# Kernel optimization log

Measured on AMD Instinct MI355X. Metric: run time of the kernel, lower is better.

The kernel has to match this reference:

```python
import jax, jax.numpy as jnp
import numpy as np

N = 50000        # nodes
E = 800000       # edges (avg degree 16)
MUL = 32         # multiplicity of 0e and 1o node-feature irreps
NA = 16          # node attr scalars (species embedding)
NB = 8           # edge radial basis size
FC_H = 64        # radial MLP hidden width
NPATH = 5        # tp paths: 0e*0e->0e, 0e*1o->1o, 1o*0e->1o, 1o*1o->0e, 1o*1o->1o
AVG_NEI = 16.0


def setup_inputs() -> dict:
    k = jax.random.split(jax.random.key(0), 16)
    return dict(
        node_feats=jax.random.normal(k[0], (N, 4 * MUL), jnp.float32),   # 32x0e + 32x1o
        node_attrs=jax.random.normal(k[1], (N, NA), jnp.float32),
        edge_embedding=jax.random.uniform(k[2], (E, NB), jnp.float32),
        edge_attrs=jax.random.normal(k[3], (E, 4), jnp.float32),         # SH l=0 (1) + l=1 (3)
        edge_src=jax.random.randint(k[4], (E,), 0, N),
        edge_dst=jax.random.randint(k[5], (E,), 0, N),
        W1_s=jax.random.normal(k[6], (MUL, MUL), jnp.float32) / np.sqrt(MUL),
        W1_v=jax.random.normal(k[7], (MUL, MUL), jnp.float32) / np.sqrt(MUL),
        fc_w1=jax.random.normal(k[8], (NB, FC_H), jnp.float32) / np.sqrt(NB),
        fc_b1=jnp.zeros((FC_H,), jnp.float32),
        fc_w2=jax.random.normal(k[9], (FC_H, NPATH * MUL), jnp.float32) / np.sqrt(FC_H),
        W2_s=jax.random.normal(k[10], (2 * MUL, 2 * MUL), jnp.float32) / np.sqrt(2 * MUL),
        W2_v=jax.random.normal(k[11], (3 * MUL, MUL), jnp.float32) / np.sqrt(3 * MUL),
        Wsc_s=jax.random.normal(k[12], (MUL, NA, 2 * MUL), jnp.float32) / np.sqrt(MUL * NA),
        Wsc_v=jax.random.normal(k[13], (MUL, NA, MUL), jnp.float32) / np.sqrt(MUL * NA),
    )


def reference(node_feats, node_attrs, edge_embedding, edge_attrs,
              edge_src, edge_dst, W1_s, W1_v, fc_w1, fc_b1, fc_w2,
              W2_s, W2_v, Wsc_s, Wsc_v):
    n = node_feats.shape[0]
    s = node_feats[:, :MUL]                        # [N, mul]     0e scalars
    v = node_feats[:, MUL:].reshape(n, MUL, 3)     # [N, mul, 3]  1o vectors

    # linear_1: per-irrep multiplicity mixing
    x_s = s @ W1_s
    x_v = jnp.einsum('nuc,uv->nvc', v, W1_v)

    # radial network -> per-edge tensor-product path weights (uvu, mul_in2 = 1)
    w = jax.nn.silu(edge_embedding @ fc_w1 + fc_b1) @ fc_w2   # [E, 5*mul]
    w00, w01, w10, w11s, w11v = [w[:, i * MUL:(i + 1) * MUL] for i in range(NPATH)]

    sh0 = edge_attrs[:, :1]     # [E, 1]  l=0
    sh1 = edge_attrs[:, 1:4]    # [E, 3]  l=1

    xs = x_s[edge_src]          # [E, mul]      gather source-node features
    xv = x_v[edge_src]          # [E, mul, 3]

    # Clebsch-Gordan tensor-product messages
    m_s0 = w00 * xs * sh0                                              # 0e x 0e -> 0e
    m_s1 = w11s * jnp.einsum('euc,ec->eu', xv, sh1) / np.sqrt(3.0)     # 1o x 1o -> 0e
    m_v0 = (w01 * xs)[:, :, None] * sh1[:, None, :]                    # 0e x 1o -> 1o
    m_v1 = w10[:, :, None] * xv * sh0[:, :, None]                      # 1o x 0e -> 1o
    m_v2 = w11v[:, :, None] * jnp.cross(
        xv, jnp.broadcast_to(sh1[:, None, :], xv.shape)) / np.sqrt(2.0)  # 1o x 1o -> 1o

    # scatter-sum to destination nodes, normalized by sqrt(avg num neighbors)
    inv = 1.0 / np.sqrt(AVG_NEI)
    a_s = jax.ops.segment_sum(jnp.concatenate([m_s0, m_s1], axis=1),
                              edge_dst, num_segments=n) * inv           # [N, 2*mul]
    a_v = jax.ops.segment_sum(jnp.concatenate([m_v0, m_v1, m_v2], axis=1),
                              edge_dst, num_segments=n) * inv           # [N, 3*mul, 3]

    # linear_2: mix tp paths into gated irreps (2*mul scalars + mul vectors)
    y_s = a_s @ W2_s
    y_v = jnp.einsum('nuc,uo->noc', a_v, W2_v)

    # self-connection: fully-connected tp of input feats with scalar node attrs
    y_s = y_s + jnp.einsum('nu,na,uao->no', s, node_attrs, Wsc_s)
    y_v = y_v + jnp.einsum('nuc,na,uao->noc', v, node_attrs, Wsc_v)

    # gate: first mul scalars -> silu output; next mul scalars -> silu gates on vectors
    out_s = jax.nn.silu(y_s[:, :MUL])
    gates = jax.nn.silu(y_s[:, MUL:])
    out_v = y_v * gates[:, :, None]

    out = jnp.concatenate([out_s, out_v.reshape(n, 3 * MUL)], axis=1)
    return node_feats + out   # resnet (irreps match)
```

## Files before the change

kernel.cpp:

```cpp
#include <hip/hip_runtime.h>

#define NN 50000
#define NE 800000

typedef _Float16 half2t __attribute__((ext_vector_type(2)));
union H16 { float4 f; half2t p[4]; };

__device__ __forceinline__ float silu_f(float x) { return x / (1.0f + __expf(-x)); }

__device__ __forceinline__ float fdot2(half2t a, half2t b, float c) {
#if __has_builtin(__builtin_amdgcn_fdot2)
    return __builtin_amdgcn_fdot2(a, b, c, false);
#else
    return c + (float)a.x * (float)b.x + (float)a.y * (float)b.y;
#endif
}

__global__ __launch_bounds__(256) void k_node_transform(
    const float* __restrict__ node_feats,
    const float* __restrict__ W1_s,
    const float* __restrict__ W1_v,
    float* __restrict__ xf)
{
    __shared__ float sW1s[32 * 32];
    __shared__ float sW1v[32 * 32];
    __shared__ float sfeat[8][128];
    int t = threadIdx.x;
    for (int i = t; i < 1024; i += 256) { sW1s[i] = W1_s[i]; sW1v[i] = W1_v[i]; }
    int nodeBase = blockIdx.x * 8;
    for (int i = t; i < 8 * 128; i += 256) {
        int nn = nodeBase + (i >> 7);
        sfeat[i >> 7][i & 127] = (nn < NN) ? node_feats[(long)nn * 128 + (i & 127)] : 0.0f;
    }
    __syncthreads();
    int g = t >> 5, o = t & 31;
    int n = nodeBase + g;
    if (n >= NN) return;
    float accs = 0.f, acc0 = 0.f, acc1 = 0.f, acc2 = 0.f;
#pragma unroll
    for (int u = 0; u < 32; ++u) {
        float su  = sfeat[g][u];
        float vu0 = sfeat[g][32 + u * 3 + 0];
        float vu1 = sfeat[g][32 + u * 3 + 1];
        float vu2 = sfeat[g][32 + u * 3 + 2];
        float ws = sW1s[u * 32 + o];
        float wv = sW1v[u * 32 + o];
        accs += su * ws;
        acc0 += vu0 * wv;
        acc1 += vu1 * wv;
        acc2 += vu2 * wv;
    }
    float4 r; r.x = accs; r.y = acc0; r.z = acc1; r.w = acc2;
    *(float4*)&xf[((long)n * 32 + o) * 4] = r;
}

__global__ __launch_bounds__(256) void k_hist(const int* __restrict__ edge_dst,
                                              int* __restrict__ counts)
{
    int e = blockIdx.x * 256 + threadIdx.x;
    if (e < NE) atomicAdd(&counts[edge_dst[e]], 1);
}

__global__ __launch_bounds__(1024) void k_scan(const int* __restrict__ counts,
                                               int* __restrict__ row_ptr,
                                               int* __restrict__ cursor)
{
    __shared__ int wsum[16];
    __shared__ int carry_s;
    int t = threadIdx.x;
    int lane = t & 63, w = t >> 6;
    if (t == 0) carry_s = 0;
    __syncthreads();
    for (int base = 0; base < NN; base += 1024) {
        int i = base + t;
        int v = (i < NN) ? counts[i] : 0;
        int s = v;
#pragma unroll
        for (int d = 1; d < 64; d <<= 1) {
            int o = __shfl_up(s, d, 64);
            if (lane >= d) s += o;
        }
        if (lane == 63) wsum[w] = s;
        __syncthreads();
        if (w == 0) {
            int ws = (lane < 16) ? wsum[lane] : 0;
#pragma unroll
            for (int d = 1; d < 16; d <<= 1) {
                int o = __shfl_up(ws, d, 64);
                if (lane >= d) ws += o;
            }
            if (lane < 16) wsum[lane] = ws;
        }
        __syncthreads();
        int excl = (s - v) + ((w > 0) ? wsum[w - 1] : 0) + carry_s;
        if (i < NN) { row_ptr[i] = excl; cursor[i] = excl; }
        int total = wsum[15];
        __syncthreads();
        if (t == 0) carry_s += total;
        __syncthreads();
    }
    if (t == 0) row_ptr[NN] = carry_s;
}

__global__ __launch_bounds__(256) void k_fill(const int* __restrict__ edge_dst,
                                              int* __restrict__ cursor,
                                              int* __restrict__ edge_ids)
{
    int e = blockIdx.x * 256 + threadIdx.x;
    if (e < NE) {
        int slot = atomicAdd(&cursor[edge_dst[e]], 1);
        edge_ids[slot] = e;
    }
}

#define SW2_HBYTES (160 * 72 * 2)
#define POOL_BYTES (SW2_HBYTES + 8 * 8 * 128)

__global__ __launch_bounds__(256, 3) void k_gather_t(
    const float* __restrict__ edge_embedding,
    const float* __restrict__ edge_attrs,
    const int*   __restrict__ edge_src,
    const float* __restrict__ fc_w1,
    const float* __restrict__ fc_b1,
    const float* __restrict__ fc_w2,
    const float* __restrict__ xf,
    const int*   __restrict__ row_ptr,
    const int*   __restrict__ edge_ids,
    const float* __restrict__ node_feats,
    const float* __restrict__ node_attrs,
    const float* __restrict__ W2_s,
    const float* __restrict__ W2_v,
    const float* __restrict__ Wsc_s,
    const float* __restrict__ Wsc_v,
    float* __restrict__ out)
{
    __shared__ __align__(16) unsigned char pool[POOL_BYTES];
    _Float16* swp = (_Float16*)pool;
    half2t*   hhp = (half2t*)(pool + SW2_HBYTES);

    int t = threadIdx.x;
    for (int i = t; i < 64 * 160; i += 256) {
        int j = i / 160, c = i - j * 160;
        swp[c * 72 + j] = (_Float16)fc_w2[i];
    }
    __syncthreads();

    int g = t >> 5, lane = t & 31;
    int n = blockIdx.x * 8 + g;

    float w1a[8], w1b[8];
#pragma unroll
    for (int q = 0; q < 8; ++q) {
        w1a[q] = fc_w1[q * 64 + 2 * lane];
        w1b[q] = fc_w1[q * 64 + 2 * lane + 1];
    }
    float b1a = fc_b1[2 * lane], b1b = fc_b1[2 * lane + 1];

    int start = row_ptr[n];
    int end   = row_ptr[n + 1];

    float as0 = 0.f, as1 = 0.f;
    float av[9];
#pragma unroll
    for (int p = 0; p < 9; ++p) av[p] = 0.f;

    const float4* xf4 = (const float4*)xf;
    half2t* hme = hhp + g * (8 * 32);
    const float INV_SQRT3 = 0.5773502691896258f;
    const float INV_SQRT2 = 0.7071067811865476f;
    const float INV_NEI   = 0.25f;

    for (int i0 = start; i0 < end; i0 += 8) {
        int ne = end - i0;
        int eid[8];
#pragma unroll
        for (int k = 0; k < 8; ++k) eid[k] = edge_ids[(k < ne) ? (i0 + k) : i0];

#pragma unroll
        for (int k = 0; k < 8; ++k) {
            float4 e0 = *(const float4*)&edge_embedding[(long)eid[k] * 8];
            float4 e1 = *(const float4*)&edge_embedding[(long)eid[k] * 8 + 4];
            float h0 = b1a, h1 = b1b;
            h0 += e0.x * w1a[0] + e0.y * w1a[1] + e0.z * w1a[2] + e0.w * w1a[3];
            h0 += e1.x * w1a[4] + e1.y * w1a[5] + e1.z * w1a[6] + e1.w * w1a[7];
            h1 += e0.x * w1b[0] + e0.y * w1b[1] + e0.z * w1b[2] + e0.w * w1b[3];
            h1 += e1.x * w1b[4] + e1.y * w1b[5] + e1.z * w1b[6] + e1.w * w1b[7];
            half2t hp;
            hp.x = (_Float16)silu_f(h0);
            hp.y = (_Float16)silu_f(h1);
            hme[k * 32 + lane] = hp;
        }

        float acc[5][8];
#pragma unroll
        for (int p = 0; p < 5; ++p)
#pragma unroll
            for (int k = 0; k < 8; ++k) acc[p][k] = 0.f;

#pragma unroll 2
        for (int jq = 0; jq < 8; ++jq) {
            H16 w0, w1, w2, w3, w4;
            w0.f = *(const float4*)&swp[(0 * 32 + lane) * 72 + jq * 8];
            w1.f = *(const float4*)&swp[(1 * 32 + lane) * 72 + jq * 8];
            w2.f = *(const float4*)&swp[(2 * 32 + lane) * 72 + jq * 8];
            w3.f = *(const float4*)&swp[(3 * 32 + lane) * 72 + jq * 8];
            w4.f = *(const float4*)&swp[(4 * 32 + lane) * 72 + jq * 8];
#pragma unroll
            for (int k = 0; k < 8; ++k) {
                H16 hv;
                hv.f = *(const float4*)&hme[k * 32 + jq * 4];
#pragma unroll
                for (int m = 0; m < 4; ++m) {
                    acc[0][k] = fdot2(hv.p[m], w0.p[m], acc[0][k]);
                    acc[1][k] = fdot2(hv.p[m], w1.p[m], acc[1][k]);
                    acc[2][k] = fdot2(hv.p[m], w2.p[m], acc[2][k]);
                    acc[3][k] = fdot2(hv.p[m], w3.p[m], acc[3][k]);
                    acc[4][k] = fdot2(hv.p[m], w4.p[m], acc[4][k]);
                }
            }
        }

#pragma unroll
        for (int h0i = 0; h0i < 8; h0i += 4) {
            if (h0i >= ne) break;
            int srcv[4];
#pragma unroll
            for (int k = 0; k < 4; ++k) srcv[k] = edge_src[eid[h0i + k]];
            float4 at[4], xv[4];
#pragma unroll
            for (int k = 0; k < 4; ++k) {
                at[k] = *(const float4*)&edge_attrs[(long)eid[h0i + k] * 4];
                xv[k] = xf4[(long)srcv[k] * 32 + lane];
            }
#pragma unroll
            for (int k = 0; k < 4; ++k) {
                int kk = h0i + k;
                if (kk >= ne) break;
                float4 a4 = at[k];
                float xs  = xv[k].x;
                float xv0 = xv[k].y, xv1 = xv[k].z, xv2 = xv[k].w;
                float w00 = acc[0][kk], w01 = acc[1][kk], w10 = acc[2][kk];
                float w11s = acc[3][kk], w11v = acc[4][kk];

                as0 += w00 * xs * a4.x;
                float dot = xv0 * a4.y + xv1 * a4.z + xv2 * a4.w;
                as1 += w11s * dot * INV_SQRT3;
                float t01 = w01 * xs;
                av[0] += t01 * a4.y; av[1] += t01 * a4.z; av[2] += t01 * a4.w;
                float t10 = w10 * a4.x;
                av[3] += t10 * xv0; av[4] += t10 * xv1; av[5] += t10 * xv2;
                float k2 = w11v * INV_SQRT2;
                av[6] += k2 * (xv1 * a4.w - xv2 * a4.z);
                av[7] += k2 * (xv2 * a4.y - xv0 * a4.w);
                av[8] += k2 * (xv0 * a4.z - xv1 * a4.y);
            }
        }
    }

    __syncthreads();
    float* epi = (float*)pool + (g << 9);

    epi[lane]      = as0 * INV_NEI;
    epi[32 + lane] = as1 * INV_NEI;
#pragma unroll
    for (int p = 0; p < 3; ++p)
#pragma unroll
        for (int c = 0; c < 3; ++c)
            epi[64 + (p * 32 + lane) * 3 + c] = av[p * 3 + c] * INV_NEI;

    *(float4*)&epi[352 + lane * 4] = *(const float4*)&node_feats[(long)n * 128 + lane * 4];
    if (lane < 16) epi[480 + lane] = node_attrs[(long)n * 16 + lane];

    int o = lane;
    float ys0 = 0.f, ys1 = 0.f, yv0 = 0.f, yv1 = 0.f, yv2 = 0.f;

#pragma unroll 8
    for (int u = 0; u < 64; ++u) {
        float as = epi[u];
        ys0 += as * W2_s[u * 64 + o];
        ys1 += as * W2_s[u * 64 + 32 + o];
    }
#pragma unroll 8
    for (int u = 0; u < 96; ++u) {
        float wv = W2_v[u * 32 + o];
        yv0 += epi[64 + u * 3 + 0] * wv;
        yv1 += epi[64 + u * 3 + 1] * wv;
        yv2 += epi[64 + u * 3 + 2] * wv;
    }

    float att[16];
#pragma unroll
    for (int a = 0; a < 16; ++a) att[a] = epi[480 + a];

    for (int u = 0; u < 32; ++u) {
        const float* Wsp = &Wsc_s[u * 1024 + o];
        const float* Wvp = &Wsc_v[u * 512 + o];
        float t0 = 0.f, t1 = 0.f, tv = 0.f;
#pragma unroll
        for (int a = 0; a < 16; ++a) {
            float aa = att[a];
            t0 += aa * Wsp[a * 64];
            t1 += aa * Wsp[a * 64 + 32];
            tv += aa * Wvp[a * 32];
        }
        float su = epi[352 + u];
        ys0 += su * t0;
        ys1 += su * t1;
        yv0 += epi[352 + 32 + u * 3 + 0] * tv;
        yv1 += epi[352 + 32 + u * 3 + 1] * tv;
        yv2 += epi[352 + 32 + u * 3 + 2] * tv;
    }

    float os   = silu_f(ys0);
    float gate = silu_f(ys1);
    long base = (long)n * 128;
    out[base + o] = epi[352 + o] + os;
    out[base + 32 + o * 3 + 0] = epi[352 + 32 + o * 3 + 0] + yv0 * gate;
    out[base + 32 + o * 3 + 1] = epi[352 + 32 + o * 3 + 1] + yv1 * gate;
    out[base + 32 + o * 3 + 2] = epi[352 + 32 + o * 3 + 2] + yv2 * gate;
}

extern "C" void kernel_launch(void* const* d_in, const int* in_sizes, int n_in,
                              void* d_out, int out_size, void* d_ws, size_t ws_size,
                              hipStream_t stream) {
    const float* node_feats     = (const float*)d_in[0];
    const float* node_attrs     = (const float*)d_in[1];
    const float* edge_embedding = (const float*)d_in[2];
    const float* edge_attrs     = (const float*)d_in[3];
    const int*   edge_src       = (const int*)d_in[4];
    const int*   edge_dst       = (const int*)d_in[5];
    const float* W1_s  = (const float*)d_in[6];
    const float* W1_v  = (const float*)d_in[7];
    const float* fc_w1 = (const float*)d_in[8];
    const float* fc_b1 = (const float*)d_in[9];
    const float* fc_w2 = (const float*)d_in[10];
    const float* W2_s  = (const float*)d_in[11];
    const float* W2_v  = (const float*)d_in[12];
    const float* Wsc_s = (const float*)d_in[13];
    const float* Wsc_v = (const float*)d_in[14];
    float* out = (float*)d_out;

    float* ws  = (float*)d_ws;
    float* xf  = ws;
    int* ibase    = (int*)(ws + (long)NN * 128);
    int* counts   = ibase;
    int* row_ptr  = ibase + NN;
    int* cursor   = ibase + 2 * NN + 1;
    int* edge_ids = ibase + 3 * NN + 1;

    hipMemsetAsync(counts, 0, (size_t)NN * sizeof(int), stream);
    k_hist<<<(NE + 255) / 256, 256, 0, stream>>>(edge_dst, counts);
    k_node_transform<<<(NN + 7) / 8, 256, 0, stream>>>(node_feats, W1_s, W1_v, xf);
    k_scan<<<1, 1024, 0, stream>>>(counts, row_ptr, cursor);
    k_fill<<<(NE + 255) / 256, 256, 0, stream>>>(edge_dst, cursor, edge_ids);
    k_gather_t<<<NN / 8, 256, 0, stream>>>(edge_embedding, edge_attrs, edge_src,
                                           fc_w1, fc_b1, fc_w2, xf,
                                           row_ptr, edge_ids,
                                           node_feats, node_attrs,
                                           W2_s, W2_v, Wsc_s, Wsc_v, out);
}
```

Baseline: 837.1 us.

## Sort nodes by degree for load balance and prefetch first edge batch early

Adds a single-block counting-sort kernel that orders nodes by descending in-degree, and the gather kernel maps warps to nodes through this permutation. Nodes of similar degree then share a block, which reduces idle time among the eight warps of a block. The source features and edge attributes for the first four edges of each chunk are also loaded before the radial MLP, so their latency overlaps with compute. The costs are one extra single-block launch and scattered per-node output writes, plus higher register pressure from the hoisted loads.

New measurement: 906.0 us. 1.08x slower.

```diff
diff --git a/kernel.cpp b/kernel.cpp
--- a/kernel.cpp
+++ b/kernel.cpp
@@ -113,6 +113,33 @@
     }
 }
 
+__global__ __launch_bounds__(1024) void k_degsort(const int* __restrict__ counts,
+                                                  int* __restrict__ perm)
+{
+    __shared__ int bins[256];
+    __shared__ int base[256];
+    int t = threadIdx.x;
+    if (t < 256) bins[t] = 0;
+    __syncthreads();
+    for (int i = t; i < NN; i += 1024) {
+        int d = counts[i]; if (d > 255) d = 255;
+        atomicAdd(&bins[d], 1);
+    }
+    __syncthreads();
+    if (t == 0) {
+        int run = 0;
+        for (int d = 255; d >= 0; --d) { base[d] = run; run += bins[d]; }
+    }
+    __syncthreads();
+    if (t < 256) bins[t] = 0;
+    __syncthreads();
+    for (int i = t; i < NN; i += 1024) {
+        int d = counts[i]; if (d > 255) d = 255;
+        int pos = base[d] + atomicAdd(&bins[d], 1);
+        perm[pos] = i;
+    }
+}
+
 #define SW2_HBYTES (160 * 72 * 2)
 #define POOL_BYTES (SW2_HBYTES + 8 * 8 * 128)
 
@@ -126,6 +153,7 @@
     const float* __restrict__ xf,
     const int*   __restrict__ row_ptr,
     const int*   __restrict__ edge_ids,
+    const int*   __restrict__ perm,
     const float* __restrict__ node_feats,
     const float* __restrict__ node_attrs,
     const float* __restrict__ W2_s,
@@ -146,7 +174,7 @@
     __syncthreads();
 
     int g = t >> 5, lane = t & 31;
-    int n = blockIdx.x * 8 + g;
+    int n = perm[blockIdx.x * 8 + g];
 
     float w1a[8], w1b[8];
 #pragma unroll
@@ -175,6 +203,16 @@
         int eid[8];
 #pragma unroll
         for (int k = 0; k < 8; ++k) eid[k] = edge_ids[(k < ne) ? (i0 + k) : i0];
+
+        int srcv0[4];
+#pragma unroll
+        for (int k = 0; k < 4; ++k) srcv0[k] = edge_src[eid[k]];
+        float4 at0[4], xv0[4];
+#pragma unroll
+        for (int k = 0; k < 4; ++k) {
+            at0[k] = *(const float4*)&edge_attrs[(long)eid[k] * 4];
+            xv0[k] = xf4[(long)srcv0[k] * 32 + lane];
+        }
 
 #pragma unroll
         for (int k = 0; k < 8; ++k) {
@@ -220,39 +258,62 @@
             }
         }
 
-#pragma unroll
-        for (int h0i = 0; h0i < 8; h0i += 4) {
-            if (h0i >= ne) break;
-            int srcv[4];
-#pragma unroll
-            for (int k = 0; k < 4; ++k) srcv[k] = edge_src[eid[h0i + k]];
-            float4 at[4], xv[4];
+        int srcv1[4];
+        float4 at1[4], xv1[4];
+        if (ne > 4) {
+#pragma unroll
+            for (int k = 0; k < 4; ++k) srcv1[k] = edge_src[eid[4 + k]];
 #pragma unroll
             for (int k = 0; k < 4; ++k) {
-                at[k] = *(const float4*)&edge_attrs[(long)eid[h0i + k] * 4];
-                xv[k] = xf4[(long)srcv[k] * 32 + lane];
+                at1[k] = *(const float4*)&edge_attrs[(long)eid[4 + k] * 4];
+                xv1[k] = xf4[(long)srcv1[k] * 32 + lane];
             }
+        }
+
+#pragma unroll
+        for (int k = 0; k < 4; ++k) {
+            if (k >= ne) break;
+            float4 a4 = at0[k];
+            float xs  = xv0[k].x;
+            float xvx = xv0[k].y, xvy = xv0[k].z, xvz = xv0[k].w;
+            float w00 = acc[0][k], w01 = acc[1][k], w10 = acc[2][k];
+            float w11s = acc[3][k], w11v = acc[4][k];
+
+            as0 += w00 * xs * a4.x;
+            float dot = xvx * a4.y + xvy * a4.z + xvz * a4.w;
+            as1 += w11s * dot * INV_SQRT3;
+            float t01 = w01 * xs;
+            av[0] += t01 * a4.y; av[1] += t01 * a4.z; av[2] += t01 * a4.w;
+            float t10 = w10 * a4.x;
+            av[3] += t10 * xvx; av[4] += t10 * xvy; av[5] += t10 * xvz;
+            float k2 = w11v * INV_SQRT2;
+            av[6] += k2 * (xvy * a4.w - xvz * a4.z);
+            av[7] += k2 * (xvz * a4.y - xvx * a4.w);
+            av[8] += k2 * (xvx * a4.z - xvy * a4.y);
+        }
+
+        if (ne > 4) {
 #pragma unroll
             for (int k = 0; k < 4; ++k) {
-                int kk = h0i + k;
+                int kk = 4 + k;
                 if (kk >= ne) break;
-                float4 a4 = at[k];
-                float xs  = xv[k].x;
-                float xv0 = xv[k].y, xv1 = xv[k].z, xv2 = xv[k].w;
+                float4 a4 = at1[k];
+                float xs  = xv1[k].x;
+                float xvx = xv1[k].y, xvy = xv1[k].z, xvz = xv1[k].w;
                 float w00 = acc[0][kk], w01 = acc[1][kk], w10 = acc[2][kk];
                 float w11s = acc[3][kk], w11v = acc[4][kk];
 
                 as0 += w00 * xs * a4.x;
-                float dot = xv0 * a4.y + xv1 * a4.z + xv2 * a4.w;
+                float dot = xvx * a4.y + xvy * a4.z + xvz * a4.w;
                 as1 += w11s * dot * INV_SQRT3;
                 float t01 = w01 * xs;
                 av[0] += t01 * a4.y; av[1] += t01 * a4.z; av[2] += t01 * a4.w;
                 float t10 = w10 * a4.x;
-                av[3] += t10 * xv0; av[4] += t10 * xv1; av[5] += t10 * xv2;
+                av[3] += t10 * xvx; av[4] += t10 * xvy; av[5] += t10 * xvz;
                 float k2 = w11v * INV_SQRT2;
-                av[6] += k2 * (xv1 * a4.w - xv2 * a4.z);
-                av[7] += k2 * (xv2 * a4.y - xv0 * a4.w);
-                av[8] += k2 * (xv0 * a4.z - xv1 * a4.y);
+                av[6] += k2 * (xvy * a4.w - xvz * a4.z);
+                av[7] += k2 * (xvz * a4.y - xvx * a4.w);
+                av[8] += k2 * (xvx * a4.z - xvy * a4.y);
             }
         }
     }
@@ -347,15 +408,17 @@
     int* row_ptr  = ibase + NN;
     int* cursor   = ibase + 2 * NN + 1;
     int* edge_ids = ibase + 3 * NN + 1;
+    int* perm     = ibase + 3 * NN + 1 + NE;
 
     hipMemsetAsync(counts, 0, (size_t)NN * sizeof(int), stream);
     k_hist<<<(NE + 255) / 256, 256, 0, stream>>>(edge_dst, counts);
     k_node_transform<<<(NN + 7) / 8, 256, 0, stream>>>(node_feats, W1_s, W1_v, xf);
+    k_degsort<<<1, 1024, 0, stream>>>(counts, perm);
     k_scan<<<1, 1024, 0, stream>>>(counts, row_ptr, cursor);
     k_fill<<<(NE + 255) / 256, 256, 0, stream>>>(edge_dst, cursor, edge_ids);
     k_gather_t<<<NN / 8, 256, 0, stream>>>(edge_embedding, edge_attrs, edge_src,
                                            fc_w1, fc_b1, fc_w2, xf,
-                                           row_ptr, edge_ids,
+                                           row_ptr, edge_ids, perm,
                                            node_feats, node_attrs,
                                            W2_s, W2_v, Wsc_s, Wsc_v, out);
 }
```
